# Kernel optimization log

Hardware: AMD Instinct MI355X
Metric: run time of the kernel (lower is better)

## Reference

```python
import jax, jax.numpy as jnp
import numpy as np

D_STATE = 16
D_CONV = 4
DT_RANK = 8


def layer_norm(x, g, b, eps=1e-5):
    m = x.mean(-1, keepdims=True)
    v = ((x - m) ** 2).mean(-1, keepdims=True)
    return (x - m) / jnp.sqrt(v + eps) * g + b


def rms_norm(x, w, eps=1e-5):
    return x * jax.lax.rsqrt(jnp.mean(x * x, -1, keepdims=True) + eps) * w


def mamba_layer(feat, in_proj_w, conv_w, conv_b, x_proj_w, dt_proj_w, dt_proj_b,
                A_log, D_param, out_proj_w, rms_w):
    # feat: [N, C] treated as a length-N sequence with batch 1 (residual block)
    x_in = rms_norm(feat, rms_w)
    xz = x_in @ in_proj_w                         # [N, 2*d_inner]
    d_inner = conv_w.shape[0]
    x, z = xz[:, :d_inner], xz[:, d_inner:]
    # causal depthwise conv1d (torch pad=d_conv-1 then truncate to L)
    L = x.shape[0]
    x_pad = jnp.pad(x, ((D_CONV - 1, 0), (0, 0)))
    xc = conv_b + sum(x_pad[k:k + L, :] * conv_w[:, k] for k in range(D_CONV))
    x = jax.nn.silu(xc)
    dbc = x @ x_proj_w                            # [N, dt_rank + 2*d_state]
    delta = jax.nn.softplus(dbc[:, :DT_RANK] @ dt_proj_w + dt_proj_b)  # [N, d_inner]
    Bm = dbc[:, DT_RANK:DT_RANK + D_STATE]        # [N, d_state]
    Cm = dbc[:, DT_RANK + D_STATE:]               # [N, d_state]
    A = -jnp.exp(A_log)                           # [d_inner, d_state]

    def step(h, inp):
        d_t, b_t, c_t, x_t = inp
        dA = jnp.exp(d_t[:, None] * A)            # [d_inner, d_state]
        h = dA * h + d_t[:, None] * b_t[None, :] * x_t[:, None]
        y_t = (h * c_t[None, :]).sum(-1)          # [d_inner]
        return h, y_t

    h0 = jnp.zeros((d_inner, D_STATE), feat.dtype)
    _, y = jax.lax.scan(step, h0, (delta, Bm, Cm, x))
    y = y + D_param * x
    y = y * jax.nn.silu(z)
    return feat + y @ out_proj_w                  # residual


def setup_inputs() -> dict:
    N, K, C = 32768, 16, 128
    d_inner = 2 * C
    key = jax.random.key(0)
    ks = jax.random.split(key, 12)
    s = 0.02
    inp = {
        "feat": jax.random.normal(ks[0], (N, C), jnp.float32),
        "coord": jax.random.normal(ks[1], (N, 3), jnp.float32),
        "reference_index": jax.random.randint(ks[2], (N, K), 0, N, jnp.int32),
        "gauss_dist": jax.random.uniform(ks[3], (N, K), jnp.float32),
        "j": 0,
        # Mamba params
        "in_proj_w": jax.random.normal(ks[4], (C, 2 * d_inner), jnp.float32) * s,
        "conv_w": jax.random.normal(ks[5], (d_inner, D_CONV), jnp.float32) * s,
        "conv_b": jnp.zeros((d_inner,), jnp.float32),
        "x_proj_w": jax.random.normal(ks[6], (d_inner, DT_RANK + 2 * D_STATE), jnp.float32) * s,
        "dt_proj_w": jax.random.normal(ks[7], (DT_RANK, d_inner), jnp.float32) * s,
        "dt_proj_b": jax.random.uniform(ks[8], (d_inner,), jnp.float32) * 0.1,
        "A_log": jnp.log(jnp.tile(jnp.arange(1.0, D_STATE + 1.0, dtype=jnp.float32), (d_inner, 1))),
        "D_param": jnp.ones((d_inner,), jnp.float32),
        "out_proj_w": jax.random.normal(ks[9], (d_inner, C), jnp.float32) * s,
        "rms_w": jnp.ones((C,), jnp.float32),
        # PointBatchNorm (LayerNorm) shared for both norms
        "ln_g": jnp.ones((C,), jnp.float32),
        "ln_b": jnp.zeros((C,), jnp.float32),
        # linear_attention: Linear(2C->C), LayerNorm, ReLU, Linear(C->C)
        "la_w1": jax.random.normal(ks[10], (2 * C, C), jnp.float32) * s,
        "la_b1": jnp.zeros((C,), jnp.float32),
        "la_ln_g": jnp.ones((C,), jnp.float32),
        "la_ln_b": jnp.zeros((C,), jnp.float32),
        "la_w2": jax.random.normal(ks[11], (C, C), jnp.float32) * s,
        "la_b2": jnp.zeros((C,), jnp.float32),
    }
    return inp


def reference(feat, coord, reference_index, gauss_dist, j,
              in_proj_w, conv_w, conv_b, x_proj_w, dt_proj_w, dt_proj_b,
              A_log, D_param, out_proj_w, rms_w, ln_g, ln_b,
              la_w1, la_b1, la_ln_g, la_ln_b, la_w2, la_b2):
    # pointops.grouping(with_xyz=False): gather neighbor features [N, K, C]
    group_feat = feat[reference_index]
    combined = (gauss_dist[..., None] * group_feat).sum(axis=1)     # [N, C]
    combined = layer_norm(combined, ln_g, ln_b)
    feat_mamba = mamba_layer(feat, in_proj_w, conv_w, conv_b, x_proj_w,
                             dt_proj_w, dt_proj_b, A_log, D_param,
                             out_proj_w, rms_w)
    feat_mamba = layer_norm(feat_mamba, ln_g, ln_b)
    cat_feat = jnp.concatenate([feat_mamba, combined], axis=-1)     # [N, 2C]
    h = jax.nn.relu(layer_norm(cat_feat @ la_w1 + la_b1, la_ln_g, la_ln_b))
    return h @ la_w2 + la_b2
```

## Files before the change

kernel.cpp:

```cpp
#include <hip/hip_runtime.h>
#include <hip/hip_bf16.h>
#include <math.h>

#define N_TOK 32768
#define LC 16
#define NCHUNK (N_TOK / LC)
#define NSEG 64
#define SEGLEN (NCHUNK / NSEG)

typedef short short8 __attribute__((ext_vector_type(8)));
typedef float f32x4 __attribute__((ext_vector_type(4)));

__device__ __forceinline__ float siluf_(float v){ return v / (1.f + __expf(-v)); }
__device__ __forceinline__ float softplusf_(float v){ return v > 20.f ? v : log1pf(__expf(v)); }

__device__ __forceinline__ unsigned f2bfu(float f){
  __hip_bfloat16 h = __float2bfloat16(f);
  return (unsigned)*(unsigned short*)&h;
}
__device__ __forceinline__ float bfu2f(unsigned short u){
  __hip_bfloat16 h; *(unsigned short*)&h = u; return __bfloat162float(h);
}

__device__ __forceinline__ float waveRed64(float v){
  #pragma unroll
  for (int m = 1; m < 64; m <<= 1) v += __shfl_xor(v, m);
  return v;
}

__device__ __forceinline__ void pow_chain(float w, float pw[16]){
  pw[0]=w; pw[1]=w*w; pw[2]=pw[1]*w; pw[3]=pw[1]*pw[1];
  pw[4]=pw[3]*pw[0]; pw[5]=pw[3]*pw[1]; pw[6]=pw[3]*pw[2]; pw[7]=pw[3]*pw[3];
  pw[8]=pw[7]*pw[0]; pw[9]=pw[7]*pw[1]; pw[10]=pw[7]*pw[2]; pw[11]=pw[7]*pw[3];
  pw[12]=pw[7]*pw[4]; pw[13]=pw[7]*pw[5]; pw[14]=pw[7]*pw[6]; pw[15]=pw[7]*pw[7];
}

__device__ __forceinline__ bool check_intA(const float aS[16]){
  bool ok = true;
  #pragma unroll
  for (int s=0;s<16;s++){
    float tgt = (float)(s+1);
    if (fabsf(-aS[s] - tgt) > 1e-4f*tgt) ok = false;
  }
  return ok;
}

__global__ void __launch_bounds__(256) k_front(const float* __restrict__ feat,
                        const int* __restrict__ ridx,
                        const float* __restrict__ gd, const float* __restrict__ g,
                        const float* __restrict__ b, const float* __restrict__ rmsw,
                        unsigned* __restrict__ catB, unsigned* __restrict__ a0u,
                        const float* __restrict__ ipw, const float* __restrict__ opw,
                        const float* __restrict__ w1, const float* __restrict__ w2,
                        const float* __restrict__ xpw,
                        __hip_bfloat16* __restrict__ ipwt, __hip_bfloat16* __restrict__ opwt,
                        __hip_bfloat16* __restrict__ w1t, __hip_bfloat16* __restrict__ w2t,
                        __hip_bfloat16* __restrict__ xpwt){
  int bid = blockIdx.x;
  if (bid >= 8192){
    int e = (bid-8192)*256 + threadIdx.x;
    if (e < 65536){ int n=e>>7, k=e&127; ipwt[e]=__float2bfloat16(ipw[k*512+n]); }
    else if (e < 98304){ int f=e-65536; int n=f>>8, k=f&255; opwt[f]=__float2bfloat16(opw[k*128+n]); }
    else if (e < 131072){ int f=e-98304; int n=f>>8, k=f&255; w1t[f]=__float2bfloat16(w1[k*128+n]); }
    else if (e < 147456){ int f=e-131072; int n=f>>7, k=f&127; w2t[f]=__float2bfloat16(w2[k*128+n]); }
    else if (e < 159744){ int f=e-147456; int n=f>>8, k=f&255;
                          xpwt[f]=(n<40)?__float2bfloat16(xpw[k*40+n]):__float2bfloat16(0.f); }
    return;
  }
  int row = bid*4 + (threadIdx.x>>6);
  int lane = threadIdx.x & 63;
  float2 f2 = ((const float2*)feat)[row*64 + lane];
  float ss = waveRed64(f2.x*f2.x + f2.y*f2.y);
  float is0 = rsqrtf(ss * (1.f/128.f) + 1e-5f);
  float2 w = ((const float2*)rmsw)[lane];
  a0u[row*64 + lane] = f2bfu(f2.x*is0*w.x) | (f2bfu(f2.y*is0*w.y) << 16);
  float ax=0.f, ay=0.f;
  #pragma unroll 4
  for (int k=0;k<16;k++){
    int idx = ridx[row*16+k];
    float ww = gd[row*16+k];
    float2 f = ((const float2*)feat)[idx*64 + lane];
    ax += ww*f.x; ay += ww*f.y;
  }
  float m = waveRed64(ax+ay) * (1.f/128.f);
  float dx = ax-m, dy = ay-m;
  float var = waveRed64(dx*dx+dy*dy) * (1.f/128.f);
  float is = rsqrtf(var + 1e-5f);
  float2 gg = ((const float2*)g)[lane];
  float2 bb = ((const float2*)b)[lane];
  float ox = dx*is*gg.x + bb.x, oy = dy*is*gg.y + bb.y;
  catB[row*64 + lane] = f2bfu(ox) | (f2bfu(oy) << 16);
}

template<int WM16, int WN16>
__global__ __launch_bounds__(256) void k_mfma(const __hip_bfloat16* __restrict__ A,
      const __hip_bfloat16* __restrict__ Wt, int K,
      __hip_bfloat16* __restrict__ out0b, __hip_bfloat16* __restrict__ out1){
  int tid = threadIdx.x;
  int wave = tid>>6, lane = tid&63;
  int wm = wave>>1, wn = wave&1;
  int lane16 = lane&15, quad = lane>>4;
  int m_w = blockIdx.x*(2*WM16*16) + wm*(WM16*16);
  int n_w = blockIdx.y*(2*WN16*16) + wn*(WN16*16);
  f32x4 acc[WM16][WN16];
  #pragma unroll
  for (int i=0;i<WM16;i++)
    #pragma unroll
    for (int j=0;j<WN16;j++) acc[i][j] = (f32x4){0.f,0.f,0.f,0.f};
  const __hip_bfloat16* Ab = A  + (size_t)(m_w + lane16)*K + quad*8;
  const __hip_bfloat16* Bb = Wt + (size_t)(n_w + lane16)*K + quad*8;
  #pragma unroll 4
  for (int kk=0; kk<K; kk+=32){
    short8 a[WM16], b[WN16];
    #pragma unroll
    for (int i=0;i<WM16;i++) a[i] = *(const short8*)(Ab + (size_t)i*16*K + kk);
    #pragma unroll
    for (int j=0;j<WN16;j++) b[j] = *(const short8*)(Bb + (size_t)j*16*K + kk);
    #pragma unroll
    for (int i=0;i<WM16;i++)
      #pragma unroll
      for (int j=0;j<WN16;j++)
        acc[i][j] = __builtin_amdgcn_mfma_f32_16x16x32_bf16(a[i], b[j], acc[i][j], 0, 0, 0);
  }
  #pragma unroll
  for (int i=0;i<WM16;i++){
    #pragma unroll
    for (int j=0;j<WN16;j++){
      int n = n_w + j*16 + lane16;
      #pragma unroll
      for (int r=0;r<4;r++){
        int m = m_w + i*16 + quad*4 + r;
        float v = acc[i][j][r];
        if (n < 256) out0b[(size_t)m*256 + n] = __float2bfloat16(v);
        else         out1[(size_t)m*256 + (n-256)] = __float2bfloat16(siluf_(v));
      }
    }
  }
}

__global__ __launch_bounds__(256) void k_xproj_mfma(const __hip_bfloat16* __restrict__ A,
      const __hip_bfloat16* __restrict__ Wt,
      float* __restrict__ dt8, float* __restrict__ Bm, float* __restrict__ Cm){
  int tid = threadIdx.x;
  int wave = tid>>6, lane = tid&63;
  int lane16 = lane&15, quad = lane>>4;
  int m_w = blockIdx.x*64 + wave*16;
  f32x4 acc[3];
  #pragma unroll
  for (int j=0;j<3;j++) acc[j] = (f32x4){0.f,0.f,0.f,0.f};
  const __hip_bfloat16* Ab = A  + (size_t)(m_w + lane16)*256 + quad*8;
  const __hip_bfloat16* Bb = Wt + (size_t)lane16*256 + quad*8;
  #pragma unroll
  for (int kk=0; kk<256; kk+=32){
    short8 a = *(const short8*)(Ab + kk);
    short8 b0 = *(const short8*)(Bb + kk);
    short8 b1 = *(const short8*)(Bb + 16*256 + kk);
    short8 b2 = *(const short8*)(Bb + 32*256 + kk);
    acc[0] = __builtin_amdgcn_mfma_f32_16x16x32_bf16(a, b0, acc[0], 0, 0, 0);
    acc[1] = __builtin_amdgcn_mfma_f32_16x16x32_bf16(a, b1, acc[1], 0, 0, 0);
    acc[2] = __builtin_amdgcn_mfma_f32_16x16x32_bf16(a, b2, acc[2], 0, 0, 0);
  }
  #pragma unroll
  for (int j=0;j<3;j++){
    int n = j*16 + lane16;
    #pragma unroll
    for (int r=0;r<4;r++){
      int m = m_w + quad*4 + r;
      float v = acc[j][r];
      if (n < 8)       dt8[(size_t)m*8 + n] = v;
      else if (n < 24) Bm[(size_t)m*16 + (n-8)] = v;
      else if (n < 40) Cm[(size_t)m*16 + (n-24)] = v;
    }
  }
}

__global__ void __launch_bounds__(256) k_conv(const __hip_bfloat16* __restrict__ bxb,
      const float* __restrict__ cw, const float* __restrict__ cb,
      __hip_bfloat16* __restrict__ xb){
  int r0 = blockIdx.x*32;
  int d = threadIdx.x;
  float w0=cw[d*4], w1=cw[d*4+1], w2=cw[d*4+2], w3=cw[d*4+3], bb=cb[d];
  float a0 = (r0 >= 3) ? __bfloat162float(bxb[(size_t)(r0-3)*256 + d]) : 0.f;
  float a1 = (r0 >= 2) ? __bfloat162float(bxb[(size_t)(r0-2)*256 + d]) : 0.f;
  float a2 = (r0 >= 1) ? __bfloat162float(bxb[(size_t)(r0-1)*256 + d]) : 0.f;
  #pragma unroll 4
  for (int t=0;t<32;t++){
    float a3 = __bfloat162float(bxb[(size_t)(r0+t)*256 + d]);
    float xc = bb + w0*a0 + w1*a1 + w2*a2 + w3*a3;
    xb[(size_t)(r0+t)*256 + d] = __float2bfloat16(siluf_(xc));
    a0=a1; a1=a2; a2=a3;
  }
}

__global__ void __launch_bounds__(256) k_delta(const float* __restrict__ dt8,
      const float* __restrict__ dtw, const float* __restrict__ dtb,
      const __hip_bfloat16* __restrict__ zb, unsigned* __restrict__ dzb){
  int row = blockIdx.x;
  int d = threadIdx.x;
  const float4* T = (const float4*)(dt8 + (size_t)row*8);
  float4 u = T[0], v = T[1];
  float acc = dtb[d]
    + u.x*dtw[0*256+d] + u.y*dtw[1*256+d] + u.z*dtw[2*256+d] + u.w*dtw[3*256+d]
    + v.x*dtw[4*256+d] + v.y*dtw[5*256+d] + v.z*dtw[6*256+d] + v.w*dtw[7*256+d];
  size_t idx = (size_t)row*256 + d;
  unsigned zu = *(const unsigned short*)&zb[idx];
  dzb[idx] = f2bfu(softplusf_(acc)) | (zu << 16);
}

__global__ __launch_bounds__(256) void k_scan1(const unsigned* __restrict__ dzb,
      const __hip_bfloat16* __restrict__ xb, const float* __restrict__ Bm,
      const float* __restrict__ A_log, float* __restrict__ dsum_o,
      __hip_bfloat16* __restrict__ Hc){
  __shared__ float Bl[LC][16];
  int g = blockIdx.x;
  int tid = threadIdx.x;
  int d = tid;
  int t0 = g*LC;
  if (tid < 64) ((float4*)&Bl[0][0])[tid] = ((const float4*)(Bm + (size_t)t0*16))[tid];
  __syncthreads();
  float aS[16];
  #pragma unroll
  for (int s=0;s<16;s++) aS[s] = -__expf(A_log[d*16+s]);
  bool fastA = check_intA(aS);
  float h[16] = {};
  float dsum = 0.f;
  if (fastA){
    #pragma unroll 4
    for (int t=0;t<LC;t++){
      unsigned u = dzb[(size_t)(t0+t)*256 + d];
      float dv = bfu2f((unsigned short)(u & 0xffff));
      float xv = __bfloat162float(xb[(size_t)(t0+t)*256 + d]);
      const float4* Bp = (const float4*)&Bl[t][0];
      float4 b0=Bp[0], b1=Bp[1], b2=Bp[2], b3=Bp[3];
      float bl[16] = {b0.x,b0.y,b0.z,b0.w, b1.x,b1.y,b1.z,b1.w,
                      b2.x,b2.y,b2.z,b2.w, b3.x,b3.y,b3.z,b3.w};
      dsum += dv;
      float dx_ = dv*xv;
      float w[16]; pow_chain(__expf(-dv), w);
      #pragma unroll
      for (int s=0;s<16;s++) h[s] = w[s]*h[s] + dx_*bl[s];
    }
  } else {
    #pragma unroll 4
    for (int t=0;t<LC;t++){
      unsigned u = dzb[(size_t)(t0+t)*256 + d];
      float dv = bfu2f((unsigned short)(u & 0xffff));
      float xv = __bfloat162float(xb[(size_t)(t0+t)*256 + d]);
      const float4* Bp = (const float4*)&Bl[t][0];
      float4 b0=Bp[0], b1=Bp[1], b2=Bp[2], b3=Bp[3];
      float bl[16] = {b0.x,b0.y,b0.z,b0.w, b1.x,b1.y,b1.z,b1.w,
                      b2.x,b2.y,b2.z,b2.w, b3.x,b3.y,b3.z,b3.w};
      dsum += dv;
      float dx_ = dv*xv;
      #pragma unroll
      for (int s=0;s<16;s++) h[s] = __expf(dv*aS[s])*h[s] + dx_*bl[s];
    }
  }
  dsum_o[(size_t)g*256 + d] = dsum;
  unsigned u[8];
  #pragma unroll
  for (int q=0;q<8;q++) u[q] = f2bfu(h[2*q]) | (f2bfu(h[2*q+1]) << 16);
  uint4* Hd = (uint4*)(Hc + (size_t)g*4096 + (size_t)d*16);
  Hd[0] = make_uint4(u[0],u[1],u[2],u[3]);
  Hd[1] = make_uint4(u[4],u[5],u[6],u[7]);
}

__global__ __launch_bounds__(256) void k_carry_a(const float* __restrict__ dsum,
      __hip_bfloat16* __restrict__ Hc, const float* __restrict__ A_log,
      float* __restrict__ dsum_pre, float* __restrict__ segsum, float* __restrict__ Hagg){
  int seg = blockIdx.x;
  int ch  = blockIdx.y*256 + threadIdx.x;
  int d = ch>>4, s = ch&15;
  float aSv = -__expf(A_log[ch]);
  float dpre = 0.f, c = 0.f;
  int g0 = seg*SEGLEN;
  #pragma unroll 4
  for (int i=0;i<SEGLEN;i++){
    int g = g0+i;
    float ds = dsum[(size_t)g*256 + d];
    size_t a = (size_t)g*4096 + ch;
    float hh = __bfloat162float(Hc[a]);
    float p = __expf(ds*aSv);
    if (s==0) dsum_pre[(size_t)g*256 + d] = dpre;
    Hc[a] = __float2bfloat16(c);
    dpre += ds;
    c = p*c + hh;
  }
  if (s==0) segsum[seg*256 + d] = dpre;
  Hagg[(size_t)seg*4096 + ch] = c;
}

__global__ __launch_bounds__(256) void k_carry_b(const float* __restrict__ segsum,
      const float* __restrict__ Hagg, const float* __restrict__ A_log,
      float* __restrict__ Cseg){
  int ch = blockIdx.x*256 + threadIdx.x;
  int d = ch>>4;
  float aSv = -__expf(A_log[ch]);
  float c = 0.f;
  #pragma unroll 8
  for (int s=0;s<NSEG;s++){
    Cseg[(size_t)s*4096 + ch] = c;
    c = __expf(segsum[s*256 + d]*aSv)*c + Hagg[(size_t)s*4096 + ch];
  }
}

__global__ __launch_bounds__(256) void k_scan2(const unsigned* __restrict__ dzb,
      const __hip_bfloat16* __restrict__ xb, const float* __restrict__ Bm,
      const float* __restrict__ Cm, const float* __restrict__ A_log,
      const float* __restrict__ Dp, const float* __restrict__ dsum_pre,
      const __hip_bfloat16* __restrict__ Hc, const float* __restrict__ Cseg,
      __hip_bfloat16* __restrict__ yb){
  __shared__ float Bl[LC][16];
  __shared__ float Cl[LC][16];
  int g = blockIdx.x;
  int tid = threadIdx.x;
  int d = tid;
  int t0 = g*LC;
  if (tid < 64) ((float4*)&Bl[0][0])[tid] = ((const float4*)(Bm + (size_t)t0*16))[tid];
  else if (tid < 128) ((float4*)&Cl[0][0])[tid-64] = ((const float4*)(Cm + (size_t)t0*16))[tid-64];
  __syncthreads();
  int seg = g / SEGLEN;
  float aS[16];
  #pragma unroll
  for (int s=0;s<16;s++) aS[s] = -__expf(A_log[d*16+s]);
  bool fastA = check_intA(aS);
  float h[16];
  {
    float dpre = dsum_pre[(size_t)g*256 + d];
    const uint4* hp = (const uint4*)(Hc + (size_t)g*4096 + (size_t)d*16);
    uint4 H0 = hp[0], H1 = hp[1];
    unsigned hu[8] = {H0.x,H0.y,H0.z,H0.w, H1.x,H1.y,H1.z,H1.w};
    const float4* cs = (const float4*)(Cseg + (size_t)seg*4096 + (size_t)d*16);
    float ws[16];
    if (fastA){
      pow_chain(__expf(-dpre), ws);
    } else {
      #pragma unroll
      for (int s=0;s<16;s++) ws[s] = __expf(dpre*aS[s]);
    }
    #pragma unroll
    for (int q=0;q<4;q++){
      float4 C = cs[q];
      h[q*4+0] = ws[q*4+0]*C.x + bfu2f((unsigned short)(hu[q*2]   & 0xffff));
      h[q*4+1] = ws[q*4+1]*C.y + bfu2f((unsigned short)(hu[q*2]   >> 16));
      h[q*4+2] = ws[q*4+2]*C.z + bfu2f((unsigned short)(hu[q*2+1] & 0xffff));
      h[q*4+3] = ws[q*4+3]*C.w + bfu2f((unsigned short)(hu[q*2+1] >> 16));
    }
  }
  float dpar = Dp[d];
  if (fastA){
    #pragma unroll 4
    for (int t=0;t<LC;t++){
      unsigned u = dzb[(size_t)(t0+t)*256 + d];
      float dv = bfu2f((unsigned short)(u & 0xffff));
      float zv = bfu2f((unsigned short)(u >> 16));
      float xv = __bfloat162float(xb[(size_t)(t0+t)*256 + d]);
      const float4* Bp = (const float4*)&Bl[t][0];
      const float4* Cp = (const float4*)&Cl[t][0];
      float4 b0=Bp[0], b1=Bp[1], b2=Bp[2], b3=Bp[3];
      float4 c0=Cp[0], c1=Cp[1], c2=Cp[2], c3=Cp[3];
      float bl[16] = {b0.x,b0.y,b0.z,b0.w, b1.x,b1.y,b1.z,b1.w,
                      b2.x,b2.y,b2.z,b2.w, b3.x,b3.y,b3.z,b3.w};
      float cl[16] = {c0.x,c0.y,c0.z,c0.w, c1.x,c1.y,c1.z,c1.w,
                      c2.x,c2.y,c2.z,c2.w, c3.x,c3.y,c3.z,c3.w};
      float dx_ = dv*xv;
      float w[16]; pow_chain(__expf(-dv), w);
      float yv = 0.f;
      #pragma unroll
      for (int s=0;s<16;s++){
        h[s] = w[s]*h[s] + dx_*bl[s];
        yv += h[s]*cl[s];
      }
      yb[(size_t)(t0+t)*256 + d] = __float2bfloat16((yv + dpar*xv)*zv);
    }
  } else {
    #pragma unroll 4
    for (int t=0;t<LC;t++){
      unsigned u = dzb[(size_t)(t0+t)*256 + d];
      float dv = bfu2f((unsigned short)(u & 0xffff));
      float zv = bfu2f((unsigned short)(u >> 16));
      float xv = __bfloat162float(xb[(size_t)(t0+t)*256 + d]);
      const float4* Bp = (const float4*)&Bl[t][0];
      const float4* Cp = (const float4*)&Cl[t][0];
      float4 b0=Bp[0], b1=Bp[1], b2=Bp[2], b3=Bp[3];
      float4 c0=Cp[0], c1=Cp[1], c2=Cp[2], c3=Cp[3];
      float bl[16] = {b0.x,b0.y,b0.z,b0.w, b1.x,b1.y,b1.z,b1.w,
                      b2.x,b2.y,b2.z,b2.w, b3.x,b3.y,b3.z,b3.w};
      float cl[16] = {c0.x,c0.y,c0.z,c0.w, c1.x,c1.y,c1.z,c1.w,
                      c2.x,c2.y,c2.z,c2.w, c3.x,c3.y,c3.z,c3.w};
      float dx_ = dv*xv;
      float yv = 0.f;
      #pragma unroll
      for (int s=0;s<16;s++){
        h[s] = __expf(dv*aS[s])*h[s] + dx_*bl[s];
        yv += h[s]*cl[s];
      }
      yb[(size_t)(t0+t)*256 + d] = __float2bfloat16((yv + dpar*xv)*zv);
    }
  }
}

__global__ __launch_bounds__(256) void k_tail(const __hip_bfloat16* __restrict__ yb,
      const __hip_bfloat16* __restrict__ opwt, const float* __restrict__ feat,
      const float* __restrict__ lng, const float* __restrict__ lnb,
      const unsigned* __restrict__ catB,
      const __hip_bfloat16* __restrict__ w1t, const float* __restrict__ b1,
      const float* __restrict__ lag, const float* __restrict__ lab,
      const __hip_bfloat16* __restrict__ w2t, const float* __restrict__ b2,
      float* __restrict__ out){
  __shared__ __align__(16) float Ls[64][132];
  __shared__ __align__(16) unsigned Cu[64][132];
  int tid = threadIdx.x;
  int wave = tid>>6, lane = tid&63;
  int wm = wave>>1, wn = wave&1;
  int lane16 = lane&15, quad = lane>>4;
  int r0 = blockIdx.x*64;

  #pragma unroll
  for (int i=0;i<16;i++){
    int idx = i*256 + tid;
    int row = idx>>6, c = idx&63;
    Cu[row][64+c] = catB[(size_t)(r0+row)*64 + c];
  }

  f32x4 acc[2][4];
  #pragma unroll
  for (int i=0;i<2;i++)
    #pragma unroll
    for (int j=0;j<4;j++) acc[i][j] = (f32x4){0.f,0.f,0.f,0.f};
  {
    const __hip_bfloat16* Ab = yb   + (size_t)(r0 + wm*32 + lane16)*256 + quad*8;
    const __hip_bfloat16* Bb = opwt + (size_t)(wn*64 + lane16)*256 + quad*8;
    #pragma unroll 2
    for (int kk=0; kk<256; kk+=32){
      short8 a[2], bf[4];
      #pragma unroll
      for (int i=0;i<2;i++) a[i] = *(const short8*)(Ab + (size_t)i*16*256 + kk);
      #pragma unroll
      for (int j=0;j<4;j++) bf[j] = *(const short8*)(Bb + (size_t)j*16*256 + kk);
      #pragma unroll
      for (int i=0;i<2;i++)
        #pragma unroll
        for (int j=0;j<4;j++)
          acc[i][j] = __builtin_amdgcn_mfma_f32_16x16x32_bf16(a[i], bf[j], acc[i][j], 0, 0, 0);
    }
  }
  #pragma unroll
  for (int i=0;i<2;i++)
    #pragma unroll
    for (int j=0;j<4;j++){
      int n = wn*64 + j*16 + lane16;
      #pragma unroll
      for (int r=0;r<4;r++){
        int m = wm*32 + i*16 + quad*4 + r;
        Ls[m][n] = acc[i][j][r] + feat[(size_t)(r0+m)*128 + n];
      }
    }
  __syncthreads();
  {
    float2 gv = ((const float2*)lng)[lane];
    float2 bv = ((const float2*)lnb)[lane];
    #pragma unroll 4
    for (int rr=0; rr<16; rr++){
      int row = wave*16 + rr;
// ... 39 lines not shown
        Ls[m][n] = acc[i][j][r] + bv1;
      }
    }
  __syncthreads();
  {
    float2 gv = ((const float2*)lag)[lane];
    float2 bv = ((const float2*)lab)[lane];
    #pragma unroll 4
    for (int rr=0; rr<16; rr++){
      int row = wave*16 + rr;
      float2 v = *(const float2*)&Ls[row][2*lane];
      float mm = waveRed64(v.x+v.y) * (1.f/128.f);
      float dx = v.x-mm, dy = v.y-mm;
      float var = waveRed64(dx*dx+dy*dy) * (1.f/128.f);
      float is = rsqrtf(var + 1e-5f);
      float ox = fmaxf(dx*is*gv.x + bv.x, 0.f);
      float oy = fmaxf(dy*is*gv.y + bv.y, 0.f);
      Cu[row][lane] = f2bfu(ox) | (f2bfu(oy) << 16);
    }
  }
  __syncthreads();
  #pragma unroll
  for (int i=0;i<2;i++)
    #pragma unroll
    for (int j=0;j<4;j++) acc[i][j] = (f32x4){0.f,0.f,0.f,0.f};
  {
    const __hip_bfloat16* Bb = w2t + (size_t)(wn*64 + lane16)*128 + quad*8;
    #pragma unroll
    for (int kk=0; kk<128; kk+=32){
      short8 a[2], bf[4];
      #pragma unroll
      for (int i=0;i<2;i++)
        a[i] = *(const short8*)(&Cu[wm*32 + i*16 + lane16][0] + (kk>>1) + quad*4);
      #pragma unroll
      for (int j=0;j<4;j++) bf[j] = *(const short8*)(Bb + (size_t)j*16*128 + kk);
      #pragma unroll
      for (int i=0;i<2;i++)
        #pragma unroll
        for (int j=0;j<4;j++)
          acc[i][j] = __builtin_amdgcn_mfma_f32_16x16x32_bf16(a[i], bf[j], acc[i][j], 0, 0, 0);
    }
  }
  #pragma unroll
  for (int i=0;i<2;i++)
    #pragma unroll
    for (int j=0;j<4;j++){
      int n = wn*64 + j*16 + lane16;
      float bv2 = b2[n];
      #pragma unroll
      for (int r=0;r<4;r++){
        int m = wm*32 + i*16 + quad*4 + r;
        out[(size_t)(r0+m)*128 + n] = acc[i][j][r] + bv2;
      }
    }
}

extern "C" void kernel_launch(void* const* d_in, const int* in_sizes, int n_in,
                              void* d_out, int out_size, void* d_ws, size_t ws_size,
                              hipStream_t stream){
  const float* feat = (const float*)d_in[0];
  const int*   ridx = (const int*)d_in[2];
  const float* gd   = (const float*)d_in[3];
  const float* ipw  = (const float*)d_in[5];
  const float* cw   = (const float*)d_in[6];
  const float* cb   = (const float*)d_in[7];
  const float* xpw  = (const float*)d_in[8];
  const float* dtw  = (const float*)d_in[9];
  const float* dtb  = (const float*)d_in[10];
  const float* alog = (const float*)d_in[11];
  const float* dpar = (const float*)d_in[12];
  const float* opw  = (const float*)d_in[13];
  const float* rmsw = (const float*)d_in[14];
  const float* lng  = (const float*)d_in[15];
  const float* lnb  = (const float*)d_in[16];
  const float* w1   = (const float*)d_in[17];
  const float* b1   = (const float*)d_in[18];
  const float* lag  = (const float*)d_in[19];
  const float* lab  = (const float*)d_in[20];
  const float* w2   = (const float*)d_in[21];
  const float* b2   = (const float*)d_in[22];
  float* out = (float*)d_out;

  char* p = (char*)d_ws;
  __hip_bfloat16* bxb  = (__hip_bfloat16*)p; p += (size_t)N_TOK*256*2;
  __hip_bfloat16* xb   = (__hip_bfloat16*)p; p += (size_t)N_TOK*256*2;
  __hip_bfloat16* zb   = (__hip_bfloat16*)p; p += (size_t)N_TOK*256*2;
  unsigned* dzb        = (unsigned*)p;       p += (size_t)N_TOK*256*4;
  unsigned* catB       = (unsigned*)p;       p += (size_t)N_TOK*64*4;
  __hip_bfloat16* yb   = (__hip_bfloat16*)p; p += (size_t)N_TOK*256*2;
  float* dt8  = (float*)p; p += (size_t)N_TOK*8*4;
  float* Bm   = (float*)p; p += (size_t)N_TOK*16*4;
  float* Cm   = (float*)p; p += (size_t)N_TOK*16*4;
  __hip_bfloat16* Hc = (__hip_bfloat16*)p; p += (size_t)NCHUNK*4096*2;
  float* dsum = (float*)p; p += (size_t)NCHUNK*256*4;
  float* dpre = (float*)p; p += (size_t)NCHUNK*256*4;
  float* segs = (float*)p; p += (size_t)NSEG*256*4;
  float* Hagg = (float*)p; p += (size_t)NSEG*4096*4;
  float* Cseg = (float*)p; p += (size_t)NSEG*4096*4;
  __hip_bfloat16* ipwt = (__hip_bfloat16*)p; p += 512*128*2;
  __hip_bfloat16* opwt = (__hip_bfloat16*)p; p += 128*256*2;
  __hip_bfloat16* w1t  = (__hip_bfloat16*)p; p += 128*256*2;
  __hip_bfloat16* w2t  = (__hip_bfloat16*)p; p += 128*128*2;
  __hip_bfloat16* xpwt = (__hip_bfloat16*)p; p += 48*256*2;
  __hip_bfloat16* a0 = yb;

  hipLaunchKernelGGL(k_front, dim3(8192+624), dim3(256), 0, stream,
                     feat, ridx, gd, lng, lnb, rmsw, catB, (unsigned*)a0,
                     ipw, opw, w1, w2, xpw, ipwt, opwt, w1t, w2t, xpwt);
  hipLaunchKernelGGL((k_mfma<4,4>), dim3(N_TOK/128, 4), dim3(256), 0, stream,
                     a0, ipwt, 128, bxb, zb);
  hipLaunchKernelGGL(k_conv,  dim3(N_TOK/32), dim3(256), 0, stream, bxb, cw, cb, xb);
  hipLaunchKernelGGL(k_xproj_mfma, dim3(N_TOK/64), dim3(256), 0, stream, xb, xpwt, dt8, Bm, Cm);
  hipLaunchKernelGGL(k_delta, dim3(N_TOK), dim3(256), 0, stream, dt8, dtw, dtb, zb, dzb);
  hipLaunchKernelGGL(k_scan1, dim3(NCHUNK), dim3(256), 0, stream,
                     dzb, xb, Bm, alog, dsum, Hc);
  hipLaunchKernelGGL(k_carry_a, dim3(NSEG, 16), dim3(256), 0, stream,
                     dsum, Hc, alog, dpre, segs, Hagg);
  hipLaunchKernelGGL(k_carry_b, dim3(16), dim3(256), 0, stream, segs, Hagg, alog, Cseg);
  hipLaunchKernelGGL(k_scan2, dim3(NCHUNK), dim3(256), 0, stream,
                     dzb, xb, Bm, Cm, alog, dpar, dpre, Hc, Cseg, yb);
  hipLaunchKernelGGL(k_tail, dim3(N_TOK/64), dim3(256), 0, stream,
                     yb, opwt, feat, lng, lnb, catB, w1t, b1, lag, lab, w2t, b2, out);
}
```

Before: 317.9 us.

## Fuse in_proj, causal conv, x_proj and delta into one LDS-staged kernel

Replaces four separate kernels (in_proj GEMM, depthwise causal conv, x_proj GEMM, delta/softplus) with a single kernel that computes each 64-row tile of in_proj (plus a 3-row halo) into shared memory, then runs conv+silu, x_proj and dt_proj in place. This removes the global round trips of bxb, xb and dt8 and packs delta with x instead of z. The scan chunk length is also doubled to halve the number of chunks. The cost is recomputing the halo rows of the in_proj GEMM and lower MFMA tiling efficiency, since each block computes only 16-row tiles against all 512 weight columns.

Result: faster. 305.5 us (-3.9%).

```diff
diff --git a/kernel.cpp b/kernel.cpp
--- a/kernel.cpp
+++ b/kernel.cpp
@@ -3,10 +3,12 @@
 #include <math.h>
 
 #define N_TOK 32768
-#define LC 16
+#define LC 32
 #define NCHUNK (N_TOK / LC)
 #define NSEG 64
 #define SEGLEN (NCHUNK / NSEG)
+#define MIDROWS 67
+#define XPAD 264
 
 typedef short short8 __attribute__((ext_vector_type(8)));
 typedef float f32x4 __attribute__((ext_vector_type(4)));
@@ -92,131 +94,138 @@
   catB[row*64 + lane] = f2bfu(ox) | (f2bfu(oy) << 16);
 }
 
-template<int WM16, int WN16>
-__global__ __launch_bounds__(256) void k_mfma(const __hip_bfloat16* __restrict__ A,
-      const __hip_bfloat16* __restrict__ Wt, int K,
-      __hip_bfloat16* __restrict__ out0b, __hip_bfloat16* __restrict__ out1){
-  int tid = threadIdx.x;
-  int wave = tid>>6, lane = tid&63;
-  int wm = wave>>1, wn = wave&1;
-  int lane16 = lane&15, quad = lane>>4;
-  int m_w = blockIdx.x*(2*WM16*16) + wm*(WM16*16);
-  int n_w = blockIdx.y*(2*WN16*16) + wn*(WN16*16);
-  f32x4 acc[WM16][WN16];
-  #pragma unroll
-  for (int i=0;i<WM16;i++)
-    #pragma unroll
-    for (int j=0;j<WN16;j++) acc[i][j] = (f32x4){0.f,0.f,0.f,0.f};
-  const __hip_bfloat16* Ab = A  + (size_t)(m_w + lane16)*K + quad*8;
-  const __hip_bfloat16* Bb = Wt + (size_t)(n_w + lane16)*K + quad*8;
-  #pragma unroll 4
-  for (int kk=0; kk<K; kk+=32){
-    short8 a[WM16], b[WN16];
-    #pragma unroll
-    for (int i=0;i<WM16;i++) a[i] = *(const short8*)(Ab + (size_t)i*16*K + kk);
-    #pragma unroll
-    for (int j=0;j<WN16;j++) b[j] = *(const short8*)(Bb + (size_t)j*16*K + kk);
-    #pragma unroll
-    for (int i=0;i<WM16;i++)
-      #pragma unroll
-      for (int j=0;j<WN16;j++)
-        acc[i][j] = __builtin_amdgcn_mfma_f32_16x16x32_bf16(a[i], b[j], acc[i][j], 0, 0, 0);
-  }
-  #pragma unroll
-  for (int i=0;i<WM16;i++){
-    #pragma unroll
-    for (int j=0;j<WN16;j++){
-      int n = n_w + j*16 + lane16;
-      #pragma unroll
-      for (int r=0;r<4;r++){
-        int m = m_w + i*16 + quad*4 + r;
-        float v = acc[i][j][r];
-        if (n < 256) out0b[(size_t)m*256 + n] = __float2bfloat16(v);
-        else         out1[(size_t)m*256 + (n-256)] = __float2bfloat16(siluf_(v));
-      }
-    }
-  }
-}
-
-__global__ __launch_bounds__(256) void k_xproj_mfma(const __hip_bfloat16* __restrict__ A,
-      const __hip_bfloat16* __restrict__ Wt,
-      float* __restrict__ dt8, float* __restrict__ Bm, float* __restrict__ Cm){
+__global__ __launch_bounds__(256) void k_mid(
+      const __hip_bfloat16* __restrict__ a0,
+      const __hip_bfloat16* __restrict__ ipwt,
+      const __hip_bfloat16* __restrict__ xpwt,
+      const float* __restrict__ cw, const float* __restrict__ cb,
+      const float* __restrict__ dtw, const float* __restrict__ dtb,
+      __hip_bfloat16* __restrict__ zb,
+      unsigned* __restrict__ dxb,
+      float* __restrict__ Bm, float* __restrict__ Cm){
+  __shared__ __align__(16) __hip_bfloat16 Xs[MIDROWS][XPAD];
+  __shared__ __align__(16) float DT[64][8];
   int tid = threadIdx.x;
   int wave = tid>>6, lane = tid&63;
   int lane16 = lane&15, quad = lane>>4;
-  int m_w = blockIdx.x*64 + wave*16;
-  f32x4 acc[3];
-  #pragma unroll
-  for (int j=0;j<3;j++) acc[j] = (f32x4){0.f,0.f,0.f,0.f};
-  const __hip_bfloat16* Ab = A  + (size_t)(m_w + lane16)*256 + quad*8;
-  const __hip_bfloat16* Bb = Wt + (size_t)lane16*256 + quad*8;
-  #pragma unroll
-  for (int kk=0; kk<256; kk+=32){
-    short8 a = *(const short8*)(Ab + kk);
-    short8 b0 = *(const short8*)(Bb + kk);
-    short8 b1 = *(const short8*)(Bb + 16*256 + kk);
-    short8 b2 = *(const short8*)(Bb + 32*256 + kk);
-    acc[0] = __builtin_amdgcn_mfma_f32_16x16x32_bf16(a, b0, acc[0], 0, 0, 0);
-    acc[1] = __builtin_amdgcn_mfma_f32_16x16x32_bf16(a, b1, acc[1], 0, 0, 0);
-    acc[2] = __builtin_amdgcn_mfma_f32_16x16x32_bf16(a, b2, acc[2], 0, 0, 0);
-  }
-  #pragma unroll
-  for (int j=0;j<3;j++){
-    int n = j*16 + lane16;
-    #pragma unroll
-    for (int r=0;r<4;r++){
-      int m = m_w + quad*4 + r;
-      float v = acc[j][r];
-      if (n < 8)       dt8[(size_t)m*8 + n] = v;
-      else if (n < 24) Bm[(size_t)m*16 + (n-8)] = v;
-      else if (n < 40) Cm[(size_t)m*16 + (n-24)] = v;
-    }
-  }
-}
-
-__global__ void __launch_bounds__(256) k_conv(const __hip_bfloat16* __restrict__ bxb,
-      const float* __restrict__ cw, const float* __restrict__ cb,
-      __hip_bfloat16* __restrict__ xb){
-  int r0 = blockIdx.x*32;
-  int d = threadIdx.x;
-  float w0=cw[d*4], w1=cw[d*4+1], w2=cw[d*4+2], w3=cw[d*4+3], bb=cb[d];
-  float a0 = (r0 >= 3) ? __bfloat162float(bxb[(size_t)(r0-3)*256 + d]) : 0.f;
-  float a1 = (r0 >= 2) ? __bfloat162float(bxb[(size_t)(r0-2)*256 + d]) : 0.f;
-  float a2 = (r0 >= 1) ? __bfloat162float(bxb[(size_t)(r0-1)*256 + d]) : 0.f;
-  #pragma unroll 4
-  for (int t=0;t<32;t++){
-    float a3 = __bfloat162float(bxb[(size_t)(r0+t)*256 + d]);
-    float xc = bb + w0*a0 + w1*a1 + w2*a2 + w3*a3;
-    xb[(size_t)(r0+t)*256 + d] = __float2bfloat16(siluf_(xc));
-    a0=a1; a1=a2; a2=a3;
-  }
-}
-
-__global__ void __launch_bounds__(256) k_delta(const float* __restrict__ dt8,
-      const float* __restrict__ dtw, const float* __restrict__ dtb,
-      const __hip_bfloat16* __restrict__ zb, unsigned* __restrict__ dzb){
-  int row = blockIdx.x;
-  int d = threadIdx.x;
-  const float4* T = (const float4*)(dt8 + (size_t)row*8);
-  float4 u = T[0], v = T[1];
-  float acc = dtb[d]
-    + u.x*dtw[0*256+d] + u.y*dtw[1*256+d] + u.z*dtw[2*256+d] + u.w*dtw[3*256+d]
-    + v.x*dtw[4*256+d] + v.y*dtw[5*256+d] + v.z*dtw[6*256+d] + v.w*dtw[7*256+d];
-  size_t idx = (size_t)row*256 + d;
-  unsigned zu = *(const unsigned short*)&zb[idx];
-  dzb[idx] = f2bfu(softplusf_(acc)) | (zu << 16);
-}
-
-__global__ __launch_bounds__(256) void k_scan1(const unsigned* __restrict__ dzb,
-      const __hip_bfloat16* __restrict__ xb, const float* __restrict__ Bm,
-      const float* __restrict__ A_log, float* __restrict__ dsum_o,
-      __hip_bfloat16* __restrict__ Hc){
+  int r0 = blockIdx.x*64;
+
+  int n_base = wave*128;
+  #pragma unroll
+  for (int i=0;i<5;i++){
+    int ldsbase = i*16;
+    int t_lane = r0 - 3 + ldsbase + lane16;
+    int tc = t_lane < 0 ? 0 : (t_lane > N_TOK-1 ? N_TOK-1 : t_lane);
+    const __hip_bfloat16* Ab = a0 + (size_t)tc*128 + quad*8;
+    short8 afr[4];
+    #pragma unroll
+    for (int k4=0;k4<4;k4++) afr[k4] = *(const short8*)(Ab + k4*32);
+    #pragma unroll
+    for (int j=0;j<8;j++){
+      int n = n_base + j*16;
+      const __hip_bfloat16* Bb = ipwt + (size_t)(n + lane16)*128 + quad*8;
+      f32x4 acc = (f32x4){0.f,0.f,0.f,0.f};
+      #pragma unroll
+      for (int k4=0;k4<4;k4++){
+        short8 bfr = *(const short8*)(Bb + k4*32);
+        acc = __builtin_amdgcn_mfma_f32_16x16x32_bf16(afr[k4], bfr, acc, 0, 0, 0);
+      }
+      int nc = n + lane16;
+      #pragma unroll
+      for (int r=0;r<4;r++){
+        int ldsrow = ldsbase + quad*4 + r;
+        int t = r0 - 3 + ldsrow;
+        float v = acc[r];
+        if (nc < 256){
+          if (ldsrow < MIDROWS)
+            Xs[ldsrow][nc] = __float2bfloat16(t < 0 ? 0.f : v);
+        } else {
+          int trel = t - r0;
+          if (trel >= 0 && trel < 64)
+            zb[(size_t)t*256 + (nc-256)] = __float2bfloat16(siluf_(v));
+        }
+      }
+    }
+  }
+  __syncthreads();
+
+  {
+    int d = tid;
+    float cw0=cw[d*4], cw1=cw[d*4+1], cw2=cw[d*4+2], cw3=cw[d*4+3], cbb=cb[d];
+    float a_0 = __bfloat162float(Xs[0][d]);
+    float a_1 = __bfloat162float(Xs[1][d]);
+    float a_2 = __bfloat162float(Xs[2][d]);
+    #pragma unroll 4
+    for (int t=0;t<64;t++){
+      float a_3 = __bfloat162float(Xs[t+3][d]);
+      float xc = siluf_(cbb + cw0*a_0 + cw1*a_1 + cw2*a_2 + cw3*a_3);
+      Xs[t+3][d] = __float2bfloat16(xc);
+      a_0=a_1; a_1=a_2; a_2=a_3;
+    }
+  }
+  __syncthreads();
+
+  {
+    int m0 = wave*16;
+    f32x4 acc3[3];
+    #pragma unroll
+    for (int j=0;j<3;j++) acc3[j] = (f32x4){0.f,0.f,0.f,0.f};
+    const __hip_bfloat16* Arow = &Xs[3 + m0 + lane16][0] + quad*8;
+    const __hip_bfloat16* Bb = xpwt + (size_t)lane16*256 + quad*8;
+    #pragma unroll
+    for (int kk=0; kk<256; kk+=32){
+      short8 a  = *(const short8*)(Arow + kk);
+      short8 b0 = *(const short8*)(Bb + kk);
+      short8 b1 = *(const short8*)(Bb + 16*256 + kk);
+      short8 b2 = *(const short8*)(Bb + 32*256 + kk);
+      acc3[0] = __builtin_amdgcn_mfma_f32_16x16x32_bf16(a, b0, acc3[0], 0, 0, 0);
+      acc3[1] = __builtin_amdgcn_mfma_f32_16x16x32_bf16(a, b1, acc3[1], 0, 0, 0);
+      acc3[2] = __builtin_amdgcn_mfma_f32_16x16x32_bf16(a, b2, acc3[2], 0, 0, 0);
+    }
+    #pragma unroll
+    for (int j=0;j<3;j++){
+      int n = j*16 + lane16;
+      #pragma unroll
+      for (int r=0;r<4;r++){
+        int m = m0 + quad*4 + r;
+        float v = acc3[j][r];
+        if (n < 8)       DT[m][n] = v;
+        else if (n < 24) Bm[(size_t)(r0+m)*16 + (n-8)] = v;
+        else if (n < 40) Cm[(size_t)(r0+m)*16 + (n-24)] = v;
+      }
+    }
+  }
+  __syncthreads();
+
+  {
+    int d = tid;
+    float w8[8];
+    #pragma unroll
+    for (int j=0;j<8;j++) w8[j] = dtw[j*256+d];
+    float dbias = dtb[d];
+    #pragma unroll 4
+    for (int t=0;t<64;t++){
+      const float4* T = (const float4*)&DT[t][0];
+      float4 u = T[0], v = T[1];
+      float acc = dbias
+        + u.x*w8[0] + u.y*w8[1] + u.z*w8[2] + u.w*w8[3]
+        + v.x*w8[4] + v.y*w8[5] + v.z*w8[6] + v.w*w8[7];
+      float dv = softplusf_(acc);
+      unsigned xu = *(const unsigned short*)&Xs[t+3][d];
+      dxb[(size_t)(r0+t)*256 + d] = f2bfu(dv) | (xu << 16);
+    }
+  }
+}
+
+__global__ __launch_bounds__(256) void k_scan1(const unsigned* __restrict__ dxb,
+      const float* __restrict__ Bm, const float* __restrict__ A_log,
+      float* __restrict__ dsum_o, __hip_bfloat16* __restrict__ Hc){
   __shared__ float Bl[LC][16];
   int g = blockIdx.x;
   int tid = threadIdx.x;
   int d = tid;
   int t0 = g*LC;
-  if (tid < 64) ((float4*)&Bl[0][0])[tid] = ((const float4*)(Bm + (size_t)t0*16))[tid];
+  if (tid < LC*4) ((float4*)&Bl[0][0])[tid] = ((const float4*)(Bm + (size_t)t0*16))[tid];
   __syncthreads();
   float aS[16];
   #pragma unroll
@@ -227,9 +236,9 @@
   if (fastA){
     #pragma unroll 4
     for (int t=0;t<LC;t++){
-      unsigned u = dzb[(size_t)(t0+t)*256 + d];
+      unsigned u = dxb[(size_t)(t0+t)*256 + d];
       float dv = bfu2f((unsigned short)(u & 0xffff));
-      float xv = __bfloat162float(xb[(size_t)(t0+t)*256 + d]);
+      float xv = bfu2f((unsigned short)(u >> 16));
       const float4* Bp = (const float4*)&Bl[t][0];
       float4 b0=Bp[0], b1=Bp[1], b2=Bp[2], b3=Bp[3];
       float bl[16] = {b0.x,b0.y,b0.z,b0.w, b1.x,b1.y,b1.z,b1.w,
@@ -243,9 +252,9 @@
   } else {
     #pragma unroll 4
     for (int t=0;t<LC;t++){
-      unsigned u = dzb[(size_t)(t0+t)*256 + d];
+      unsigned u = dxb[(size_t)(t0+t)*256 + d];
       float dv = bfu2f((unsigned short)(u & 0xffff));
-      float xv = __bfloat162float(xb[(size_t)(t0+t)*256 + d]);
+      float xv = bfu2f((unsigned short)(u >> 16));
       const float4* Bp = (const float4*)&Bl[t][0];
       float4 b0=Bp[0], b1=Bp[1], b2=Bp[2], b3=Bp[3];
       float bl[16] = {b0.x,b0.y,b0.z,b0.w, b1.x,b1.y,b1.z,b1.w,
@@ -304,8 +313,8 @@
   }
 }
 
-__global__ __launch_bounds__(256) void k_scan2(const unsigned* __restrict__ dzb,
-      const __hip_bfloat16* __restrict__ xb, const float* __restrict__ Bm,
+__global__ __launch_bounds__(256) void k_scan2(const unsigned* __restrict__ dxb,
+      const __hip_bfloat16* __restrict__ zb, const float* __restrict__ Bm,
       const float* __restrict__ Cm, const float* __restrict__ A_log,
       const float* __restrict__ Dp, const float* __restrict__ dsum_pre,
       const __hip_bfloat16* __restrict__ Hc, const float* __restrict__ Cseg,
@@ -316,8 +325,8 @@
   int tid = threadIdx.x;
   int d = tid;
   int t0 = g*LC;
-  if (tid < 64) ((float4*)&Bl[0][0])[tid] = ((const float4*)(Bm + (size_t)t0*16))[tid];
-  else if (tid < 128) ((float4*)&Cl[0][0])[tid-64] = ((const float4*)(Cm + (size_t)t0*16))[tid-64];
+  if (tid < 128) ((float4*)&Bl[0][0])[tid] = ((const float4*)(Bm + (size_t)t0*16))[tid];
+  else ((float4*)&Cl[0][0])[tid-128] = ((const float4*)(Cm + (size_t)t0*16))[tid-128];
   __syncthreads();
   int seg = g / SEGLEN;
   float aS[16];
@@ -351,10 +360,10 @@
   if (fastA){
     #pragma unroll 4
     for (int t=0;t<LC;t++){
-      unsigned u = dzb[(size_t)(t0+t)*256 + d];
+      unsigned u = dxb[(size_t)(t0+t)*256 + d];
       float dv = bfu2f((unsigned short)(u & 0xffff));
-      float zv = bfu2f((unsigned short)(u >> 16));
-      float xv = __bfloat162float(xb[(size_t)(t0+t)*256 + d]);
+      float xv = bfu2f((unsigned short)(u >> 16));
+      float zv = __bfloat162float(zb[(size_t)(t0+t)*256 + d]);
       const float4* Bp = (const float4*)&Bl[t][0];
       const float4* Cp = (const float4*)&Cl[t][0];
       float4 b0=Bp[0], b1=Bp[1], b2=Bp[2], b3=Bp[3];
@@ -376,10 +385,10 @@
   } else {
     #pragma unroll 4
     for (int t=0;t<LC;t++){
-      unsigned u = dzb[(size_t)(t0+t)*256 + d];
+      unsigned u = dxb[(size_t)(t0+t)*256 + d];
       float dv = bfu2f((unsigned short)(u & 0xffff));
-      float zv = bfu2f((unsigned short)(u >> 16));
-      float xv = __bfloat162float(xb[(size_t)(t0+t)*256 + d]);
+      float xv = bfu2f((unsigned short)(u >> 16));
+      float zv = __bfloat162float(zb[(size_t)(t0+t)*256 + d]);
       const float4* Bp = (const float4*)&Bl[t][0];
       const float4* Cp = (const float4*)&Cl[t][0];
       float4 b0=Bp[0], b1=Bp[1], b2=Bp[2], b3=Bp[3];
@@ -585,13 +594,10 @@
   float* out = (float*)d_out;
 
   char* p = (char*)d_ws;
-  __hip_bfloat16* bxb  = (__hip_bfloat16*)p; p += (size_t)N_TOK*256*2;
-  __hip_bfloat16* xb   = (__hip_bfloat16*)p; p += (size_t)N_TOK*256*2;
   __hip_bfloat16* zb   = (__hip_bfloat16*)p; p += (size_t)N_TOK*256*2;
-  unsigned* dzb        = (unsigned*)p;       p += (size_t)N_TOK*256*4;
+  unsigned* dxb        = (unsigned*)p;       p += (size_t)N_TOK*256*4;
   unsigned* catB       = (unsigned*)p;       p += (size_t)N_TOK*64*4;
   __hip_bfloat16* yb   = (__hip_bfloat16*)p; p += (size_t)N_TOK*256*2;
-  float* dt8  = (float*)p; p += (size_t)N_TOK*8*4;
   float* Bm   = (float*)p; p += (size_t)N_TOK*16*4;
   float* Cm   = (float*)p; p += (size_t)N_TOK*16*4;
   __hip_bfloat16* Hc = (__hip_bfloat16*)p; p += (size_t)NCHUNK*4096*2;
@@ -610,18 +616,15 @@
   hipLaunchKernelGGL(k_front, dim3(8192+624), dim3(256), 0, stream,
                      feat, ridx, gd, lng, lnb, rmsw, catB, (unsigned*)a0,
                      ipw, opw, w1, w2, xpw, ipwt, opwt, w1t, w2t, xpwt);
-  hipLaunchKernelGGL((k_mfma<4,4>), dim3(N_TOK/128, 4), dim3(256), 0, stream,
-                     a0, ipwt, 128, bxb, zb);
-  hipLaunchKernelGGL(k_conv,  dim3(N_TOK/32), dim3(256), 0, stream, bxb, cw, cb, xb);
-  hipLaunchKernelGGL(k_xproj_mfma, dim3(N_TOK/64), dim3(256), 0, stream, xb, xpwt, dt8, Bm, Cm);
-  hipLaunchKernelGGL(k_delta, dim3(N_TOK), dim3(256), 0, stream, dt8, dtw, dtb, zb, dzb);
+  hipLaunchKernelGGL(k_mid, dim3(N_TOK/64), dim3(256), 0, stream,
+                     a0, ipwt, xpwt, cw, cb, dtw, dtb, zb, dxb, Bm, Cm);
   hipLaunchKernelGGL(k_scan1, dim3(NCHUNK), dim3(256), 0, stream,
-                     dzb, xb, Bm, alog, dsum, Hc);
+                     dxb, Bm, alog, dsum, Hc);
   hipLaunchKernelGGL(k_carry_a, dim3(NSEG, 16), dim3(256), 0, stream,
                      dsum, Hc, alog, dpre, segs, Hagg);
   hipLaunchKernelGGL(k_carry_b, dim3(16), dim3(256), 0, stream, segs, Hagg, alog, Cseg);
   hipLaunchKernelGGL(k_scan2, dim3(NCHUNK), dim3(256), 0, stream,
-                     dzb, xb, Bm, Cm, alog, dpar, dpre, Hc, Cseg, yb);
+                     dxb, zb, Bm, Cm, alog, dpar, dpre, Hc, Cseg, yb);
   hipLaunchKernelGGL(k_tail, dim3(N_TOK/64), dim3(256), 0, stream,
                      yb, opwt, feat, lng, lnb, catB, w1t, b1, lag, lab, w2t, b2, out);
 }
```

## Double scan chunk length and pack delta with x instead of z

Applied to the files above, without the earlier changes.

Scan chunks grow from 16 to 32 tokens, which halves the number of chunk states written to Hc and processed by the carry kernels, at the cost of a longer serial loop per block and half as many blocks. The packed 32-bit buffer now pairs delta with x rather than z. scan1 therefore reads a single array instead of two, while scan2 still reads the packed word plus z. The B/C shared-memory loads are resized to match the new chunk length.

After: 313.4 us. No clear change (-1.4%).

```diff
diff --git a/kernel.cpp b/kernel.cpp
--- a/kernel.cpp
+++ b/kernel.cpp
@@ -3,7 +3,7 @@
 #include <math.h>
 
 #define N_TOK 32768
-#define LC 16
+#define LC 32
 #define NCHUNK (N_TOK / LC)
 #define NSEG 64
 #define SEGLEN (NCHUNK / NSEG)
@@ -138,42 +138,6 @@
   }
 }
 
-__global__ __launch_bounds__(256) void k_xproj_mfma(const __hip_bfloat16* __restrict__ A,
-      const __hip_bfloat16* __restrict__ Wt,
-      float* __restrict__ dt8, float* __restrict__ Bm, float* __restrict__ Cm){
-  int tid = threadIdx.x;
-  int wave = tid>>6, lane = tid&63;
-  int lane16 = lane&15, quad = lane>>4;
-  int m_w = blockIdx.x*64 + wave*16;
-  f32x4 acc[3];
-  #pragma unroll
-  for (int j=0;j<3;j++) acc[j] = (f32x4){0.f,0.f,0.f,0.f};
-  const __hip_bfloat16* Ab = A  + (size_t)(m_w + lane16)*256 + quad*8;
-  const __hip_bfloat16* Bb = Wt + (size_t)lane16*256 + quad*8;
-  #pragma unroll
-  for (int kk=0; kk<256; kk+=32){
-    short8 a = *(const short8*)(Ab + kk);
-    short8 b0 = *(const short8*)(Bb + kk);
-    short8 b1 = *(const short8*)(Bb + 16*256 + kk);
-    short8 b2 = *(const short8*)(Bb + 32*256 + kk);
-    acc[0] = __builtin_amdgcn_mfma_f32_16x16x32_bf16(a, b0, acc[0], 0, 0, 0);
-    acc[1] = __builtin_amdgcn_mfma_f32_16x16x32_bf16(a, b1, acc[1], 0, 0, 0);
-    acc[2] = __builtin_amdgcn_mfma_f32_16x16x32_bf16(a, b2, acc[2], 0, 0, 0);
-  }
-  #pragma unroll
-  for (int j=0;j<3;j++){
-    int n = j*16 + lane16;
-    #pragma unroll
-    for (int r=0;r<4;r++){
-      int m = m_w + quad*4 + r;
-      float v = acc[j][r];
-      if (n < 8)       dt8[(size_t)m*8 + n] = v;
-      else if (n < 24) Bm[(size_t)m*16 + (n-8)] = v;
-      else if (n < 40) Cm[(size_t)m*16 + (n-24)] = v;
-    }
-  }
-}
-
 __global__ void __launch_bounds__(256) k_conv(const __hip_bfloat16* __restrict__ bxb,
       const float* __restrict__ cw, const float* __restrict__ cb,
       __hip_bfloat16* __restrict__ xb){
@@ -192,9 +156,45 @@
   }
 }
 
+__global__ __launch_bounds__(256) void k_xproj_mfma(const __hip_bfloat16* __restrict__ A,
+      const __hip_bfloat16* __restrict__ Wt,
+      float* __restrict__ dt8, float* __restrict__ Bm, float* __restrict__ Cm){
+  int tid = threadIdx.x;
+  int wave = tid>>6, lane = tid&63;
+  int lane16 = lane&15, quad = lane>>4;
+  int m_w = blockIdx.x*64 + wave*16;
+  f32x4 acc[3];
+  #pragma unroll
+  for (int j=0;j<3;j++) acc[j] = (f32x4){0.f,0.f,0.f,0.f};
+  const __hip_bfloat16* Ab = A  + (size_t)(m_w + lane16)*256 + quad*8;
+  const __hip_bfloat16* Bb = Wt + (size_t)lane16*256 + quad*8;
+  #pragma unroll
+  for (int kk=0; kk<256; kk+=32){
+    short8 a = *(const short8*)(Ab + kk);
+    short8 b0 = *(const short8*)(Bb + kk);
+    short8 b1 = *(const short8*)(Bb + 16*256 + kk);
+    short8 b2 = *(const short8*)(Bb + 32*256 + kk);
+    acc[0] = __builtin_amdgcn_mfma_f32_16x16x32_bf16(a, b0, acc[0], 0, 0, 0);
+    acc[1] = __builtin_amdgcn_mfma_f32_16x16x32_bf16(a, b1, acc[1], 0, 0, 0);
+    acc[2] = __builtin_amdgcn_mfma_f32_16x16x32_bf16(a, b2, acc[2], 0, 0, 0);
+  }
+  #pragma unroll
+  for (int j=0;j<3;j++){
+    int n = j*16 + lane16;
+    #pragma unroll
+    for (int r=0;r<4;r++){
+      int m = m_w + quad*4 + r;
+      float v = acc[j][r];
+      if (n < 8)       dt8[(size_t)m*8 + n] = v;
+      else if (n < 24) Bm[(size_t)m*16 + (n-8)] = v;
+      else if (n < 40) Cm[(size_t)m*16 + (n-24)] = v;
+    }
+  }
+}
+
 __global__ void __launch_bounds__(256) k_delta(const float* __restrict__ dt8,
       const float* __restrict__ dtw, const float* __restrict__ dtb,
-      const __hip_bfloat16* __restrict__ zb, unsigned* __restrict__ dzb){
+      const __hip_bfloat16* __restrict__ xb, unsigned* __restrict__ dxb){
   int row = blockIdx.x;
   int d = threadIdx.x;
   const float4* T = (const float4*)(dt8 + (size_t)row*8);
@@ -203,20 +203,19 @@
     + u.x*dtw[0*256+d] + u.y*dtw[1*256+d] + u.z*dtw[2*256+d] + u.w*dtw[3*256+d]
     + v.x*dtw[4*256+d] + v.y*dtw[5*256+d] + v.z*dtw[6*256+d] + v.w*dtw[7*256+d];
   size_t idx = (size_t)row*256 + d;
-  unsigned zu = *(const unsigned short*)&zb[idx];
-  dzb[idx] = f2bfu(softplusf_(acc)) | (zu << 16);
-}
-
-__global__ __launch_bounds__(256) void k_scan1(const unsigned* __restrict__ dzb,
-      const __hip_bfloat16* __restrict__ xb, const float* __restrict__ Bm,
-      const float* __restrict__ A_log, float* __restrict__ dsum_o,
-      __hip_bfloat16* __restrict__ Hc){
+  unsigned xu = *(const unsigned short*)&xb[idx];
+  dxb[idx] = f2bfu(softplusf_(acc)) | (xu << 16);
+}
+
+__global__ __launch_bounds__(256) void k_scan1(const unsigned* __restrict__ dxb,
+      const float* __restrict__ Bm, const float* __restrict__ A_log,
+      float* __restrict__ dsum_o, __hip_bfloat16* __restrict__ Hc){
   __shared__ float Bl[LC][16];
   int g = blockIdx.x;
   int tid = threadIdx.x;
   int d = tid;
   int t0 = g*LC;
-  if (tid < 64) ((float4*)&Bl[0][0])[tid] = ((const float4*)(Bm + (size_t)t0*16))[tid];
+  if (tid < LC*4) ((float4*)&Bl[0][0])[tid] = ((const float4*)(Bm + (size_t)t0*16))[tid];
   __syncthreads();
   float aS[16];
   #pragma unroll
@@ -227,9 +226,9 @@
   if (fastA){
     #pragma unroll 4
     for (int t=0;t<LC;t++){
-      unsigned u = dzb[(size_t)(t0+t)*256 + d];
+      unsigned u = dxb[(size_t)(t0+t)*256 + d];
       float dv = bfu2f((unsigned short)(u & 0xffff));
-      float xv = __bfloat162float(xb[(size_t)(t0+t)*256 + d]);
+      float xv = bfu2f((unsigned short)(u >> 16));
       const float4* Bp = (const float4*)&Bl[t][0];
       float4 b0=Bp[0], b1=Bp[1], b2=Bp[2], b3=Bp[3];
       float bl[16] = {b0.x,b0.y,b0.z,b0.w, b1.x,b1.y,b1.z,b1.w,
@@ -243,9 +242,9 @@
   } else {
     #pragma unroll 4
     for (int t=0;t<LC;t++){
-      unsigned u = dzb[(size_t)(t0+t)*256 + d];
+      unsigned u = dxb[(size_t)(t0+t)*256 + d];
       float dv = bfu2f((unsigned short)(u & 0xffff));
-      float xv = __bfloat162float(xb[(size_t)(t0+t)*256 + d]);
+      float xv = bfu2f((unsigned short)(u >> 16));
       const float4* Bp = (const float4*)&Bl[t][0];
       float4 b0=Bp[0], b1=Bp[1], b2=Bp[2], b3=Bp[3];
       float bl[16] = {b0.x,b0.y,b0.z,b0.w, b1.x,b1.y,b1.z,b1.w,
@@ -304,8 +303,8 @@
   }
 }
 
-__global__ __launch_bounds__(256) void k_scan2(const unsigned* __restrict__ dzb,
-      const __hip_bfloat16* __restrict__ xb, const float* __restrict__ Bm,
+__global__ __launch_bounds__(256) void k_scan2(const unsigned* __restrict__ dxb,
+      const __hip_bfloat16* __restrict__ zb, const float* __restrict__ Bm,
       const float* __restrict__ Cm, const float* __restrict__ A_log,
       const float* __restrict__ Dp, const float* __restrict__ dsum_pre,
       const __hip_bfloat16* __restrict__ Hc, const float* __restrict__ Cseg,
@@ -316,8 +315,8 @@
   int tid = threadIdx.x;
   int d = tid;
   int t0 = g*LC;
-  if (tid < 64) ((float4*)&Bl[0][0])[tid] = ((const float4*)(Bm + (size_t)t0*16))[tid];
-  else if (tid < 128) ((float4*)&Cl[0][0])[tid-64] = ((const float4*)(Cm + (size_t)t0*16))[tid-64];
+  if (tid < 128) ((float4*)&Bl[0][0])[tid] = ((const float4*)(Bm + (size_t)t0*16))[tid];
+  else ((float4*)&Cl[0][0])[tid-128] = ((const float4*)(Cm + (size_t)t0*16))[tid-128];
   __syncthreads();
   int seg = g / SEGLEN;
   float aS[16];
@@ -351,10 +350,10 @@
   if (fastA){
     #pragma unroll 4
     for (int t=0;t<LC;t++){
-      unsigned u = dzb[(size_t)(t0+t)*256 + d];
+      unsigned u = dxb[(size_t)(t0+t)*256 + d];
       float dv = bfu2f((unsigned short)(u & 0xffff));
-      float zv = bfu2f((unsigned short)(u >> 16));
-      float xv = __bfloat162float(xb[(size_t)(t0+t)*256 + d]);
+      float xv = bfu2f((unsigned short)(u >> 16));
+      float zv = __bfloat162float(zb[(size_t)(t0+t)*256 + d]);
       const float4* Bp = (const float4*)&Bl[t][0];
       const float4* Cp = (const float4*)&Cl[t][0];
       float4 b0=Bp[0], b1=Bp[1], b2=Bp[2], b3=Bp[3];
@@ -376,10 +375,10 @@
   } else {
     #pragma unroll 4
     for (int t=0;t<LC;t++){
-      unsigned u = dzb[(size_t)(t0+t)*256 + d];
+      unsigned u = dxb[(size_t)(t0+t)*256 + d];
       float dv = bfu2f((unsigned short)(u & 0xffff));
-      float zv = bfu2f((unsigned short)(u >> 16));
-      float xv = __bfloat162float(xb[(size_t)(t0+t)*256 + d]);
+      float xv = bfu2f((unsigned short)(u >> 16));
+      float zv = __bfloat162float(zb[(size_t)(t0+t)*256 + d]);
       const float4* Bp = (const float4*)&Bl[t][0];
       const float4* Cp = (const float4*)&Cl[t][0];
       float4 b0=Bp[0], b1=Bp[1], b2=Bp[2], b3=Bp[3];
@@ -588,7 +587,7 @@
   __hip_bfloat16* bxb  = (__hip_bfloat16*)p; p += (size_t)N_TOK*256*2;
   __hip_bfloat16* xb   = (__hip_bfloat16*)p; p += (size_t)N_TOK*256*2;
   __hip_bfloat16* zb   = (__hip_bfloat16*)p; p += (size_t)N_TOK*256*2;
-  unsigned* dzb        = (unsigned*)p;       p += (size_t)N_TOK*256*4;
+  unsigned* dxb        = (unsigned*)p;       p += (size_t)N_TOK*256*4;
   unsigned* catB       = (unsigned*)p;       p += (size_t)N_TOK*64*4;
   __hip_bfloat16* yb   = (__hip_bfloat16*)p; p += (size_t)N_TOK*256*2;
   float* dt8  = (float*)p; p += (size_t)N_TOK*8*4;
@@ -614,14 +613,14 @@
                      a0, ipwt, 128, bxb, zb);
   hipLaunchKernelGGL(k_conv,  dim3(N_TOK/32), dim3(256), 0, stream, bxb, cw, cb, xb);
   hipLaunchKernelGGL(k_xproj_mfma, dim3(N_TOK/64), dim3(256), 0, stream, xb, xpwt, dt8, Bm, Cm);
-  hipLaunchKernelGGL(k_delta, dim3(N_TOK), dim3(256), 0, stream, dt8, dtw, dtb, zb, dzb);
+  hipLaunchKernelGGL(k_delta, dim3(N_TOK), dim3(256), 0, stream, dt8, dtw, dtb, xb, dxb);
   hipLaunchKernelGGL(k_scan1, dim3(NCHUNK), dim3(256), 0, stream,
-                     dzb, xb, Bm, alog, dsum, Hc);
+                     dxb, Bm, alog, dsum, Hc);
   hipLaunchKernelGGL(k_carry_a, dim3(NSEG, 16), dim3(256), 0, stream,
                      dsum, Hc, alog, dpre, segs, Hagg);
   hipLaunchKernelGGL(k_carry_b, dim3(16), dim3(256), 0, stream, segs, Hagg, alog, Cseg);
   hipLaunchKernelGGL(k_scan2, dim3(NCHUNK), dim3(256), 0, stream,
-                     dzb, xb, Bm, Cm, alog, dpar, dpre, Hc, Cseg, yb);
+                     dxb, zb, Bm, Cm, alog, dpar, dpre, Hc, Cseg, yb);
   hipLaunchKernelGGL(k_tail, dim3(N_TOK/64), dim3(256), 0, stream,
                      yb, opwt, feat, lng, lnb, catB, w1t, b1, lag, lab, w2t, b2, out);
 }
```
